# Kernel optimization log

Hardware: AMD Instinct MI355X
Metric: run time of the kernel (lower is better)

The kernel has to match this reference:

```python
import jax, jax.numpy as jnp
import numpy as np

T, B, N, E, NF, L = 4, 8, 5000, 80000, 16, 3


def setup_inputs() -> dict:
    key = jax.random.key(0)
    ks = jax.random.split(key, 12)
    xs = jax.random.normal(ks[0], (T, B, N, 3), jnp.float32)
    vs = jax.random.normal(ks[1], (T, B, N, 3), jnp.float32)
    charges = jax.random.uniform(ks[2], (B * N, 1), jnp.float32)
    edge_src = jax.random.randint(ks[3], (E,), 0, N)
    edge_dst = jax.random.randint(ks[4], (E,), 0, N)
    theta = jax.random.uniform(ks[5], (1, T), jnp.float32, -1.0, 1.0)  # uniform_(-1,1)
    W_embed = jax.random.normal(ks[6], (1, NF), jnp.float32) * 0.5
    W1 = jax.random.normal(ks[7], (L, 2 * NF + 1, NF), jnp.float32) / jnp.sqrt(2.0 * NF + 1)
    b1 = jnp.zeros((L, NF), jnp.float32)
    W2 = jax.random.normal(ks[8], (L, NF, NF), jnp.float32) / jnp.sqrt(float(NF))
    b2 = jnp.zeros((L, NF), jnp.float32)
    Wv = jax.random.normal(ks[9], (L, NF, 1), jnp.float32) * 0.1
    return dict(xs=xs, vs=vs, charges=charges, edge_src=edge_src, edge_dst=edge_dst,
                theta=theta, W_embed=W_embed, W1=W1, b1=b1, W2=W2, b2=b2, Wv=Wv)


def reference(xs, vs, charges, edge_src, edge_dst, theta, W_embed, W1, b1, W2, b2, Wv):
    T_, B_, N_, _ = xs.shape
    # node scalar features ('f' / type-0) initialized from charges
    h0 = jax.nn.relu(charges.reshape(B_, N_, 1) @ W_embed)  # [B, N, NF]

    def graph_step(x, v, h):
        # x, v: [N,3]; h: [N,NF]. Equivariant message passing with edge rel-pos gather.
        d = x[edge_dst] - x[edge_src]                      # [E,3]  (edata['d'])
        d2 = jnp.sum(d * d, axis=-1, keepdims=True)        # [E,1]  invariant edge feature
        vec = v                                            # type-1 ('vel') channel
        for l in range(L):
            feat = jnp.concatenate([h[edge_src], h[edge_dst], d2], axis=-1)  # [E,2NF+1]
            m = jax.nn.relu(feat @ W1[l] + b1[l])                            # [E,NF]
            agg = jax.ops.segment_sum(m, edge_dst, num_segments=N_)          # [N,NF]
            h = h + jax.nn.relu(agg @ W2[l] + b2[l])
            # equivariant vector update: scatter d-weighted messages
            vec = vec + jax.ops.segment_sum(d * (m @ Wv[l]), edge_dst, num_segments=N_)
        return vec + x  # module returns out + xs

    step_b = jax.vmap(graph_step)                                  # over batch
    out = jax.vmap(lambda x, v: step_b(x, v, h0))(xs, vs)          # [T,B,N,3]
    x = out.reshape(T_, B_ * N_, 3)                                # step's view(-1, 3)
    x_hat = jnp.einsum('ij,jkt->ikt', jax.nn.softmax(theta, axis=1), x)
    return x_hat.squeeze(0)  # [B*N, 3] since num_future == 1
```

## Files before the change

kernel.cpp:

```cpp
#include <hip/hip_runtime.h>
#include <hip/hip_bf16.h>

constexpr int T_ = 4;
constexpr int B_ = 8;
constexpr int N_ = 5000;
constexpr int E_ = 80000;
constexpr int TBN = T_ * B_ * N_;
constexpr int NXCD = 8;
constexpr int CAP = 64;

constexpr int NPB = 32;
constexpr int CH  = (N_ + NPB - 1) / NPB;
constexpr int GRP = T_ * B_ / NXCD;
constexpr int LB  = NXCD * CH * GRP;
constexpr int EB  = (E_ + 255) / 256;
constexpr int IB  = TBN / 256;


__device__ __forceinline__ unsigned bf16pack2(float lo, float hi) {
    unsigned ul = (__float_as_uint(lo) + 0x8000u) >> 16;
    unsigned uh = (__float_as_uint(hi) + 0x8000u) & 0xffff0000u;
    return uh | ul;
}
__device__ __forceinline__ void bf16unpack2(unsigned u, float& lo, float& hi) {
    lo = __uint_as_float(u << 16);
    hi = __uint_as_float(u & 0xffff0000u);
}

__global__ void k_build(const int* __restrict__ src, const int* __restrict__ dst,
                        int* __restrict__ cursor, int* __restrict__ csr_b,
                        const float* __restrict__ xs, const float* __restrict__ vs,
                        const float* __restrict__ charges,
                        float4* __restrict__ rec0, float4* __restrict__ rec1,
                        float* __restrict__ vec) {
    const int bid = blockIdx.x;
    const int tid = threadIdx.x;
    if (bid < EB) {
        int e = bid * 256 + tid;
        if (e < E_) {
            int d = dst[e];
            int pos = atomicAdd(&cursor[d], 1);
            if (pos < CAP) csr_b[d * CAP + pos] = src[e];
        }
    } else {
        int g = (bid - EB) * 256 + tid;
        int tb = g / N_;
        int n  = g - tb * N_;
        int b  = tb % B_;
        float c = charges[b * N_ + n];
        float4 xc = make_float4(xs[3*(size_t)g], xs[3*(size_t)g+1], xs[3*(size_t)g+2], c);
        rec0[(size_t)g * 3 + 2] = xc;
        rec1[(size_t)g * 3 + 2] = xc;
        vec[3*(size_t)g+0] = vs[3*(size_t)g+0];
        vec[3*(size_t)g+1] = vs[3*(size_t)g+1];
        vec[3*(size_t)g+2] = vs[3*(size_t)g+2];
    }
}

template <int LYR, bool HAS_NEXT>
__global__ __launch_bounds__(256, 6) void k_layer(
        const float4* __restrict__ rec_in, float4* __restrict__ rec_out,
        const float* __restrict__ W_embed,
        const float* __restrict__ W1, const float* __restrict__ b1,
        const float* __restrict__ W2, const float* __restrict__ b2,
        const float* __restrict__ Wv,
        const int* __restrict__ degv, const int* __restrict__ csr_b,
        float* __restrict__ h, unsigned* __restrict__ gd,
        float* __restrict__ vec) {
    __shared__ float s_w1e[16], s_wv[16], s_b2[16], s_b1[16], s_b1n[16];
    __shared__ float s_W2[256];
    __shared__ float s_W1sn[256];
    __shared__ float s_W1dn[256];
    __shared__ float s_P[16], s_Q[16], s_rwe[16];
    const int tid = threadIdx.x;
    if (tid < 16) {
        s_w1e[tid] = W1[LYR * 528 + 512 + tid];
        s_wv[tid]  = Wv[LYR * 16 + tid];
        s_b2[tid]  = b2[LYR * 16 + tid];
        s_b1[tid]  = b1[LYR * 16 + tid];
        if (HAS_NEXT) s_b1n[tid] = b1[(LYR + 1) * 16 + tid];
    }
    s_W2[tid] = W2[LYR * 256 + tid];
    if (HAS_NEXT) {
        s_W1sn[tid] = W1[(LYR + 1) * 528 + tid];
        s_W1dn[tid] = W1[(LYR + 1) * 528 + 256 + tid];
    }
    if (LYR == 0 && tid < 16) {
        float accP = 0.0f, accQ = 0.0f;
        for (int j = 0; j < 16; ++j) {
            float r = fmaxf(W_embed[j], 0.0f);
            accP += r * W1[j * 16 + tid];
            accQ += r * W1[256 + j * 16 + tid];
        }
        s_P[tid] = accP; s_Q[tid] = accQ;
        s_rwe[tid] = fmaxf(W_embed[tid], 0.0f);
    }
    __syncthreads();

    const int bid   = blockIdx.x;
    const int xcd   = bid & 7;
    const int j     = bid >> 3;
    const int tb    = xcd + NXCD * (j / CH);
    const int chunk = j % CH;
    const int o     = tid & 7;
    const int node  = chunk * NPB + (tid >> 3);
    const int half  = o & 1;
    const int pr    = o >> 1;
    const int hb    = half * 8;
    if (node >= N_) return;

    const int g = tb * N_ + node;
    const size_t nb = (size_t)tb * N_;
    const uint4* r4 = (const uint4*)rec_in;

    const float4 xn = rec_in[(size_t)g * 3 + 2];
    const float c0 = xn.w;

    float gdn[8];
    if (LYR == 0) {
#pragma unroll
        for (int k = 0; k < 8; ++k) gdn[k] = c0 * s_Q[hb + k] + s_b1[hb + k];
    } else {
        uint4 da = ((const uint4*)gd)[(size_t)g * 2 + half];
        bf16unpack2(da.x, gdn[0], gdn[1]);  bf16unpack2(da.y, gdn[2], gdn[3]);
        bf16unpack2(da.z, gdn[4], gdn[5]);  bf16unpack2(da.w, gdn[6], gdn[7]);
    }

    float agg[8];
#pragma unroll
    for (int k = 0; k < 8; ++k) agg[k] = 0.0f;
    float av0 = 0.0f, av1 = 0.0f, av2 = 0.0f;

    const int deg = min(degv[node], CAP);
    const int rs = node * CAP;
    const int re = rs + deg;

    int e = rs + pr;
    bool have = e < re;
    int s = have ? csr_b[e] : 0;
    size_t si = nb + (size_t)s;
    float4 xc = rec_in[si * 3 + 2];
    uint4  ga;
    if (LYR != 0) ga = r4[si * 3 + half];

    while (have) {
        int e2 = e + 4;
        bool have2 = e2 < re;
        int s2 = have2 ? csr_b[e2] : 0;
        size_t si2 = nb + (size_t)s2;
        float4 xc2 = rec_in[si2 * 3 + 2];
        uint4  ga2;
        if (LYR != 0) ga2 = r4[si2 * 3 + half];

        float d0 = xn.x - xc.x;
        float d1 = xn.y - xc.y;
        float d2v = xn.z - xc.z;
        float dd = d0*d0 + d1*d1 + d2v*d2v;

        float gsf[8];
        if (LYR == 0) {
            float cs = xc.w;
#pragma unroll
            for (int k = 0; k < 8; ++k) gsf[k] = cs * s_P[hb + k];
        } else {
            bf16unpack2(ga.x, gsf[0], gsf[1]);  bf16unpack2(ga.y, gsf[2], gsf[3]);
            bf16unpack2(ga.z, gsf[4], gsf[5]);  bf16unpack2(ga.w, gsf[6], gsf[7]);
        }

        float sval = 0.0f;
#pragma unroll
        for (int k = 0; k < 8; ++k) {
            float mv = fmaxf(__builtin_fmaf(dd, s_w1e[hb + k], gdn[k]) + gsf[k], 0.0f);
            if (HAS_NEXT) agg[k] += mv;
            sval = __builtin_fmaf(mv, s_wv[hb + k], sval);
        }
        sval += __shfl_xor(sval, 1);
        av0 = __builtin_fmaf(d0, sval, av0);
        av1 = __builtin_fmaf(d1, sval, av1);
        av2 = __builtin_fmaf(d2v, sval, av2);

        e = e2; have = have2; xc = xc2; ga = ga2;
    }

    av0 += __shfl_xor(av0, 2); av0 += __shfl_xor(av0, 4);
    av1 += __shfl_xor(av1, 2); av1 += __shfl_xor(av1, 4);
    av2 += __shfl_xor(av2, 2); av2 += __shfl_xor(av2, 4);

    if (o < 3) {
        float myav = (o == 0) ? av0 : ((o == 1) ? av1 : av2);
        vec[(size_t)g * 3 + o] += myav;
    }

    if (HAS_NEXT) {
#pragma unroll
        for (int k = 0; k < 8; ++k) {
            agg[k] += __shfl_xor(agg[k], 2);
            agg[k] += __shfl_xor(agg[k], 4);
        }
        float aggO[8];
#pragma unroll
        for (int k = 0; k < 8; ++k) aggO[k] = __shfl_xor(agg[k], 1);
        const int j0 = hb;
        const int j1 = 8 - hb;

        float hq0, hq1;
        if (LYR == 0) {
            hq0 = c0 * s_rwe[o * 2];
            hq1 = c0 * s_rwe[o * 2 + 1];
        } else {
            float2 hv = ((const float2*)h)[(size_t)g * 8 + o];
            hq0 = hv.x; hq1 = hv.y;
        }

        float a0 = s_b2[o * 2], a1 = s_b2[o * 2 + 1];
#pragma unroll
        for (int k = 0; k < 8; ++k) {
            a0 = __builtin_fmaf(agg[k],  s_W2[(j0 + k) * 16 + o * 2],     a0);
            a1 = __builtin_fmaf(agg[k],  s_W2[(j0 + k) * 16 + o * 2 + 1], a1);
            a0 = __builtin_fmaf(aggO[k], s_W2[(j1 + k) * 16 + o * 2],     a0);
            a1 = __builtin_fmaf(aggO[k], s_W2[(j1 + k) * 16 + o * 2 + 1], a1);
        }
        hq0 += fmaxf(a0, 0.0f);
        hq1 += fmaxf(a1, 0.0f);

        const int lane = tid & 63;
        const int lbase = lane & ~7;
        float hfull[16];
#pragma unroll
        for (int sq = 0; sq < 8; ++sq) {
            hfull[sq * 2]     = __shfl(hq0, lbase + sq, 64);
            hfull[sq * 2 + 1] = __shfl(hq1, lbase + sq, 64);
        }

        float gs0 = 0.0f, gs1 = 0.0f;
        float gd0 = s_b1n[o * 2], gd1 = s_b1n[o * 2 + 1];
#pragma unroll
        for (int jj = 0; jj < 16; ++jj) {
            float hj = hfull[jj];
            gs0 = __builtin_fmaf(hj, s_W1sn[jj * 16 + o * 2],     gs0);
            gs1 = __builtin_fmaf(hj, s_W1sn[jj * 16 + o * 2 + 1], gs1);
            gd0 = __builtin_fmaf(hj, s_W1dn[jj * 16 + o * 2],     gd0);
            gd1 = __builtin_fmaf(hj, s_W1dn[jj * 16 + o * 2 + 1], gd1);
        }

        ((float2*)h)[(size_t)g * 8 + o] = make_float2(hq0, hq1);
        ((unsigned*)rec_out)[(size_t)g * 12 + o] = bf16pack2(gs0, gs1);
        ((unsigned*)gd)[(size_t)g * 8 + o]       = bf16pack2(gd0, gd1);
    }
}

__global__ void k_final(const float* __restrict__ xs, const float* __restrict__ vec,
                        const float* __restrict__ theta, float* __restrict__ out) {
    int g = blockIdx.x * 256 + threadIdx.x;
    if (g >= B_ * N_) return;
    float t0 = theta[0], t1 = theta[1], t2 = theta[2], t3 = theta[3];
    float mx = fmaxf(fmaxf(t0, t1), fmaxf(t2, t3));
    float e0 = expf(t0 - mx), e1 = expf(t1 - mx), e2 = expf(t2 - mx), e3 = expf(t3 - mx);
    float is = 1.0f / (e0 + e1 + e2 + e3);
    float w[4] = {e0 * is, e1 * is, e2 * is, e3 * is};

    int b = g / N_;
    int n = g - b * N_;
    float o0 = 0.0f, o1 = 0.0f, o2 = 0.0f;
#pragma unroll
    for (int t = 0; t < 4; ++t) {
        size_t idx = ((size_t)(t * B_ + b) * N_ + n) * 3;
        o0 += w[t] * (vec[idx+0] + xs[idx+0]);
        o1 += w[t] * (vec[idx+1] + xs[idx+1]);
        o2 += w[t] * (vec[idx+2] + xs[idx+2]);
    }
    out[(size_t)g*3+0] = o0;
    out[(size_t)g*3+1] = o1;
    out[(size_t)g*3+2] = o2;
}

extern "C" void kernel_launch(void* const* d_in, const int* in_sizes, int n_in,
                              void* d_out, int out_size, void* d_ws, size_t ws_size,
                              hipStream_t stream) {
    const float* xs       = (const float*)d_in[0];
    const float* vs       = (const float*)d_in[1];
    const float* charges  = (const float*)d_in[2];
    const int*   edge_src = (const int*)d_in[3];
    const int*   edge_dst = (const int*)d_in[4];
    const float* theta    = (const float*)d_in[5];
    const float* W_embed  = (const float*)d_in[6];
    const float* W1       = (const float*)d_in[7];
    const float* b1       = (const float*)d_in[8];
    const float* W2       = (const float*)d_in[9];
    const float* b2       = (const float*)d_in[10];
    const float* Wv       = (const float*)d_in[11];
    float* out = (float*)d_out;

    char* w = (char*)d_ws;
    size_t off = 0;
    auto take = [&](size_t bytes) {
        size_t o = off;
        off = (off + bytes + 255) & ~(size_t)255;
        return o;
    };
    int*      cursor    = (int*)(w + take((size_t)N_ * 4));
    int*      csr_b     = (int*)(w + take((size_t)N_ * CAP * 4));
    float4*   rec0      = (float4*)(w + take((size_t)TBN * 48));
    float4*   rec1      = (float4*)(w + take((size_t)TBN * 48));
    float*    h         = (float*)(w + take((size_t)TBN * 16 * 4));
    unsigned* gd        = (unsigned*)(w + take((size_t)TBN * 32));
    float*    vec       = (float*)(w + take((size_t)TBN * 3 * 4));
    (void)ws_size;

    hipMemsetAsync(cursor, 0, (size_t)N_ * 4, stream);
    k_build<<<EB + IB, 256, 0, stream>>>(edge_src, edge_dst, cursor, csr_b,
                                         xs, vs, charges, rec0, rec1, vec);

    k_layer<0, true ><<<LB, 256, 0, stream>>>(rec0, rec1, W_embed, W1, b1, W2, b2, Wv,
                                              cursor, csr_b, h, gd, vec);
    k_layer<1, true ><<<LB, 256, 0, stream>>>(rec1, rec0, W_embed, W1, b1, W2, b2, Wv,
                                              cursor, csr_b, h, gd, vec);
    k_layer<2, false><<<LB, 256, 0, stream>>>(rec0, nullptr, W_embed, W1, b1, W2, b2, Wv,
                                              cursor, csr_b, h, gd, vec);

    const int fb = (B_ * N_ + 255) / 256;
    k_final<<<fb, 256, 0, stream>>>(xs, vec, theta, out);
}
```

Before: 105.5 us.

## Fuse final softmax-weighted reduction into last layer and shrink CSR and hidden buffers

Removes the separate final kernel: the last layer computes the softmax time weight and atomically accumulates weighted vec+x into a zeroed output. CSR source indices are stored as 16-bit values and the hidden state is stored packed as bf16, reducing memory traffic. In exchange it adds an output memset, float atomics with nondeterministic summation order, and reduced hidden-state precision.

Result: no change. 106.8 us (+1.2%).

```diff
diff --git a/kernel.cpp b/kernel.cpp
--- a/kernel.cpp
+++ b/kernel.cpp
@@ -28,7 +28,7 @@
 }
 
 __global__ void k_build(const int* __restrict__ src, const int* __restrict__ dst,
-                        int* __restrict__ cursor, int* __restrict__ csr_b,
+                        int* __restrict__ cursor, unsigned short* __restrict__ csr_b,
                         const float* __restrict__ xs, const float* __restrict__ vs,
                         const float* __restrict__ charges,
                         float4* __restrict__ rec0, float4* __restrict__ rec1,
@@ -40,7 +40,7 @@
         if (e < E_) {
             int d = dst[e];
             int pos = atomicAdd(&cursor[d], 1);
-            if (pos < CAP) csr_b[d * CAP + pos] = src[e];
+            if (pos < CAP) csr_b[d * CAP + pos] = (unsigned short)src[e];
         }
     } else {
         int g = (bid - EB) * 256 + tid;
@@ -63,10 +63,10 @@
         const float* __restrict__ W_embed,
         const float* __restrict__ W1, const float* __restrict__ b1,
         const float* __restrict__ W2, const float* __restrict__ b2,
-        const float* __restrict__ Wv,
-        const int* __restrict__ degv, const int* __restrict__ csr_b,
-        float* __restrict__ h, unsigned* __restrict__ gd,
-        float* __restrict__ vec) {
+        const float* __restrict__ Wv, const float* __restrict__ theta,
+        const int* __restrict__ degv, const unsigned short* __restrict__ csr_b,
+        unsigned* __restrict__ hbuf, unsigned* __restrict__ gd,
+        float* __restrict__ vec, float* __restrict__ outp) {
     __shared__ float s_w1e[16], s_wv[16], s_b2[16], s_b1[16], s_b1n[16];
     __shared__ float s_W2[256];
     __shared__ float s_W1sn[256];
@@ -113,6 +113,17 @@
     const size_t nb = (size_t)tb * N_;
     const uint4* r4 = (const uint4*)rec_in;
 
+    float wsm = 0.0f;
+    if (!HAS_NEXT) {
+        float t0 = theta[0], t1 = theta[1], t2 = theta[2], t3 = theta[3];
+        float mx = fmaxf(fmaxf(t0, t1), fmaxf(t2, t3));
+        float e0 = expf(t0 - mx), e1 = expf(t1 - mx);
+        float e2 = expf(t2 - mx), e3 = expf(t3 - mx);
+        float inv = 1.0f / (e0 + e1 + e2 + e3);
+        int tt = tb >> 3;
+        wsm = ((tt == 0) ? e0 : (tt == 1) ? e1 : (tt == 2) ? e2 : e3) * inv;
+    }
+
     const float4 xn = rec_in[(size_t)g * 3 + 2];
     const float c0 = xn.w;
 
@@ -137,7 +148,7 @@
 
     int e = rs + pr;
     bool have = e < re;
-    int s = have ? csr_b[e] : 0;
+    int s = have ? (int)csr_b[e] : 0;
     size_t si = nb + (size_t)s;
     float4 xc = rec_in[si * 3 + 2];
     uint4  ga;
@@ -146,7 +157,7 @@
     while (have) {
         int e2 = e + 4;
         bool have2 = e2 < re;
-        int s2 = have2 ? csr_b[e2] : 0;
+        int s2 = have2 ? (int)csr_b[e2] : 0;
         size_t si2 = nb + (size_t)s2;
         float4 xc2 = rec_in[si2 * 3 + 2];
         uint4  ga2;
@@ -186,12 +197,12 @@
     av1 += __shfl_xor(av1, 2); av1 += __shfl_xor(av1, 4);
     av2 += __shfl_xor(av2, 2); av2 += __shfl_xor(av2, 4);
 
-    if (o < 3) {
-        float myav = (o == 0) ? av0 : ((o == 1) ? av1 : av2);
-        vec[(size_t)g * 3 + o] += myav;
-    }
-
     if (HAS_NEXT) {
+        if (o < 3) {
+            float myav = (o == 0) ? av0 : ((o == 1) ? av1 : av2);
+            vec[(size_t)g * 3 + o] += myav;
+        }
+
 #pragma unroll
         for (int k = 0; k < 8; ++k) {
             agg[k] += __shfl_xor(agg[k], 2);
@@ -208,8 +219,7 @@
             hq0 = c0 * s_rwe[o * 2];
             hq1 = c0 * s_rwe[o * 2 + 1];
         } else {
-            float2 hv = ((const float2*)h)[(size_t)g * 8 + o];
-            hq0 = hv.x; hq1 = hv.y;
+            bf16unpack2(hbuf[(size_t)g * 8 + o], hq0, hq1);
         }
 
         float a0 = s_b2[o * 2], a1 = s_b2[o * 2 + 1];
@@ -243,35 +253,19 @@
             gd1 = __builtin_fmaf(hj, s_W1dn[jj * 16 + o * 2 + 1], gd1);
         }
 
-        ((float2*)h)[(size_t)g * 8 + o] = make_float2(hq0, hq1);
+        hbuf[(size_t)g * 8 + o] = bf16pack2(hq0, hq1);
         ((unsigned*)rec_out)[(size_t)g * 12 + o] = bf16pack2(gs0, gs1);
         ((unsigned*)gd)[(size_t)g * 8 + o]       = bf16pack2(gd0, gd1);
-    }
-}
-
-__global__ void k_final(const float* __restrict__ xs, const float* __restrict__ vec,
-                        const float* __restrict__ theta, float* __restrict__ out) {
-    int g = blockIdx.x * 256 + threadIdx.x;
-    if (g >= B_ * N_) return;
-    float t0 = theta[0], t1 = theta[1], t2 = theta[2], t3 = theta[3];
-    float mx = fmaxf(fmaxf(t0, t1), fmaxf(t2, t3));
-    float e0 = expf(t0 - mx), e1 = expf(t1 - mx), e2 = expf(t2 - mx), e3 = expf(t3 - mx);
-    float is = 1.0f / (e0 + e1 + e2 + e3);
-    float w[4] = {e0 * is, e1 * is, e2 * is, e3 * is};
-
-    int b = g / N_;
-    int n = g - b * N_;
-    float o0 = 0.0f, o1 = 0.0f, o2 = 0.0f;
-#pragma unroll
-    for (int t = 0; t < 4; ++t) {
-        size_t idx = ((size_t)(t * B_ + b) * N_ + n) * 3;
-        o0 += w[t] * (vec[idx+0] + xs[idx+0]);
-        o1 += w[t] * (vec[idx+1] + xs[idx+1]);
-        o2 += w[t] * (vec[idx+2] + xs[idx+2]);
-    }
-    out[(size_t)g*3+0] = o0;
-    out[(size_t)g*3+1] = o1;
-    out[(size_t)g*3+2] = o2;
+    } else {
+        if (o < 3) {
+            float myav = (o == 0) ? av0 : ((o == 1) ? av1 : av2);
+            float xno  = (o == 0) ? xn.x : ((o == 1) ? xn.y : xn.z);
+            float prev = vec[(size_t)g * 3 + o];
+            int b = tb & 7;
+            atomicAdd(&outp[((size_t)b * N_ + node) * 3 + o],
+                      wsm * (prev + myav + xno));
+        }
+    }
 }
 
 extern "C" void kernel_launch(void* const* d_in, const int* in_sizes, int n_in,
@@ -298,26 +292,24 @@
         off = (off + bytes + 255) & ~(size_t)255;
         return o;
     };
-    int*      cursor    = (int*)(w + take((size_t)N_ * 4));
-    int*      csr_b     = (int*)(w + take((size_t)N_ * CAP * 4));
-    float4*   rec0      = (float4*)(w + take((size_t)TBN * 48));
-    float4*   rec1      = (float4*)(w + take((size_t)TBN * 48));
-    float*    h         = (float*)(w + take((size_t)TBN * 16 * 4));
-    unsigned* gd        = (unsigned*)(w + take((size_t)TBN * 32));
-    float*    vec       = (float*)(w + take((size_t)TBN * 3 * 4));
+    int*            cursor = (int*)(w + take((size_t)N_ * 4));
+    unsigned short* csr_b  = (unsigned short*)(w + take((size_t)N_ * CAP * 2));
+    float4*         rec0   = (float4*)(w + take((size_t)TBN * 48));
+    float4*         rec1   = (float4*)(w + take((size_t)TBN * 48));
+    unsigned*       hbuf   = (unsigned*)(w + take((size_t)TBN * 32));
+    unsigned*       gd     = (unsigned*)(w + take((size_t)TBN * 32));
+    float*          vec    = (float*)(w + take((size_t)TBN * 3 * 4));
     (void)ws_size;
 
     hipMemsetAsync(cursor, 0, (size_t)N_ * 4, stream);
+    hipMemsetAsync(out, 0, (size_t)out_size * 4, stream);
     k_build<<<EB + IB, 256, 0, stream>>>(edge_src, edge_dst, cursor, csr_b,
                                          xs, vs, charges, rec0, rec1, vec);
 
     k_layer<0, true ><<<LB, 256, 0, stream>>>(rec0, rec1, W_embed, W1, b1, W2, b2, Wv,
-                                              cursor, csr_b, h, gd, vec);
+                                              theta, cursor, csr_b, hbuf, gd, vec, out);
     k_layer<1, true ><<<LB, 256, 0, stream>>>(rec1, rec0, W_embed, W1, b1, W2, b2, Wv,
-                                              cursor, csr_b, h, gd, vec);
+                                              theta, cursor, csr_b, hbuf, gd, vec, out);
     k_layer<2, false><<<LB, 256, 0, stream>>>(rec0, nullptr, W_embed, W1, b1, W2, b2, Wv,
-                                              cursor, csr_b, h, gd, vec);
-
-    const int fb = (B_ * N_ + 255) / 256;
-    k_final<<<fb, 256, 0, stream>>>(xs, vec, theta, out);
-}
+                                              theta, cursor, csr_b, hbuf, gd, vec, out);
+}
```
